# Performance work log

Measured on AMD Instinct MI355X. Metric: run time of the kernel, lower is better.

The kernel has to match this reference:

```python
import jax, jax.numpy as jnp
import numpy as np

B, T, E, H, DL, CC, K = 64, 2048, 512, 128, 1024, 32, 31


def setup_inputs() -> dict:
    key = jax.random.key(0)
    ks = jax.random.split(key, 8)
    return {
        "encoder_output": jax.random.normal(ks[0], (B, T, E), jnp.float32),
        "processed_encoder_output": jax.random.normal(ks[1], (B, T, H), jnp.float32),
        "lstm_output": jax.random.normal(ks[2], (B, 1, DL), jnp.float32),
        "attention_weights_cum": jax.random.uniform(ks[3], (B, T), jnp.float32),
        # learned params (torch Linear stores [out, in]; y = x @ W.T)
        "W_lstm": jax.random.normal(ks[4], (H, DL), jnp.float32) * 0.02,
        "conv_w": jax.random.normal(ks[5], (CC, 1, K), jnp.float32) * 0.1,
        "W_loc": jax.random.normal(ks[6], (H, CC), jnp.float32) * 0.1,
        "W_e": jax.random.normal(ks[7], (1, H), jnp.float32) * 0.1,
    }


def _forward(encoder_output, processed_encoder_output, lstm_output,
             attention_weights_cum, W_lstm, conv_w, W_loc, W_e):
    # [B,1,1024] @ [1024,128] -> [B,1,128]
    processed_lstm = jnp.einsum('bqd,hd->bqh', lstm_output, W_lstm)
    # location conv: [B,1,T] -> [B,32,T], same padding
    loc = lax.conv_general_dilated(
        attention_weights_cum[:, None, :], conv_w,
        window_strides=(1,), padding=[(K // 2, K // 2)],
        dimension_numbers=('NCH', 'OIH', 'NCH'))
    # transpose to [B,T,32] then dense to [B,T,128]
    processed_attn = jnp.einsum('bct,hc->bth', loc, W_loc)
    # additive energies: [B,T,128] -> [B,T]
    energies = jnp.einsum('bth,oh->bto',
                          jnp.tanh(processed_lstm + processed_attn + processed_encoder_output),
                          W_e)[..., 0]
    attention_weights = jax.nn.softmax(energies, axis=1)  # [B,T]
    # bmm: [B,1,T] @ [B,T,E] -> [B,1,E]
    attention_context = jnp.einsum('bt,bte->be', attention_weights, encoder_output)[:, None, :]
    return attention_context, attention_weights

from jax import lax


def reference(encoder_output, processed_encoder_output, lstm_output,
              attention_weights_cum, W_lstm, conv_w, W_loc, W_e):
    return _forward(encoder_output, processed_encoder_output, lstm_output,
                    attention_weights_cum, W_lstm, conv_w, W_loc, W_e)
```

## Files before the change

### kernel.cpp

```cpp
#include <hip/hip_runtime.h>
#include <math.h>


#define BB 64
#define TT 2048
#define EE 512
#define HH 128
#define DLL 1024
#define CCC 32
#define KK 31

#define WS_FW   0
#define WS_PL   4096
#define WS_EN   12288
#define WS_ST   143360
#define WS_PART 145472

__global__ __launch_bounds__(256) void k0_prep(const float* __restrict__ lstm,
                                               const float* __restrict__ Wl,
                                               const float* __restrict__ cw,
                                               const float* __restrict__ Wloc,
                                               float* __restrict__ ws) {
  const int blk = blockIdx.x;
  const int tid = threadIdx.x;
  if (blk < 2048) {
    const int wave = tid >> 6, lane = tid & 63;
    const int wg = blk * 4 + wave;
    const int b = wg >> 7, h = wg & 127;
    const float4* wr = (const float4*)(Wl + (size_t)h * DLL);
    const float4* lr = (const float4*)(lstm + (size_t)b * DLL);
    float s = 0.f;
#pragma unroll
    for (int m = 0; m < 4; ++m) {
      float4 a = wr[m * 64 + lane];
      float4 c = lr[m * 64 + lane];
      s += a.x * c.x + a.y * c.y + a.z * c.z + a.w * c.w;
    }
#pragma unroll
    for (int m = 1; m < 64; m <<= 1) s += __shfl_xor(s, m, 64);
    if (lane == 0) ws[WS_PL + b * HH + h] = s;
  } else {
    __shared__ __align__(16) float wl_s[HH * CCC];
    __shared__ __align__(16) float cw_s[CCC * KK];
#pragma unroll
    for (int m = 0; m < 4; ++m)
      ((float4*)wl_s)[tid + 256 * m] = ((const float4*)Wloc)[tid + 256 * m];
    if (tid < 248) ((float4*)cw_s)[tid] = ((const float4*)cw)[tid];
    __syncthreads();
    const int h = tid >> 1;
    const int kbase = (tid & 1) * 16;
    const int kn = (tid & 1) ? 15 : 16;
    for (int kk = 0; kk < kn; ++kk) {
      const int k = kbase + kk;
      float s = 0.f;
#pragma unroll
      for (int c = 0; c < CCC; ++c) s += wl_s[h * CCC + c] * cw_s[c * KK + k];
      ws[WS_FW + h * 32 + k] = s;
    }
    if (tid & 1) ws[WS_FW + h * 32 + 31] = 0.f;
  }
}

__global__ __launch_bounds__(256) void k1_fused(const float* __restrict__ pe,
                                                const float* __restrict__ aw,
                                                const float* __restrict__ We,
                                                const float* __restrict__ enc,
                                                float* __restrict__ ws) {
  const int b = blockIdx.y;
  const int chunk = blockIdx.x;
  const int t0 = chunk * 128;
  const int tid = threadIdx.x;
  const int wave = tid >> 6, lane = tid & 63;

  __shared__ __align__(16) float aw_s[160];
  __shared__ __align__(16) float e_s[128];
  __shared__ __align__(16) float w_chunk[128];
  __shared__ __align__(16) float4 acc_s[128];
  __shared__ float sm[4], ss[4], mb_s;

  if (tid < 160) {
    const int tg = t0 - 16 + tid;
    aw_s[tid] = (tg >= 0 && tg < TT) ? aw[b * TT + tg] : 0.f;
  }

  const int h0 = 2 * lane;
  float fw0[32], fw1[32];
  {
    const float4* f4 = (const float4*)(ws + WS_FW);
#pragma unroll
    for (int m = 0; m < 8; ++m) {
      float4 a = f4[h0 * 8 + m];
      fw0[4 * m + 0] = a.x; fw0[4 * m + 1] = a.y;
      fw0[4 * m + 2] = a.z; fw0[4 * m + 3] = a.w;
      float4 c = f4[h0 * 8 + 8 + m];
      fw1[4 * m + 0] = c.x; fw1[4 * m + 1] = c.y;
      fw1[4 * m + 2] = c.z; fw1[4 * m + 3] = c.w;
    }
  }
  const float2 plv = ((const float2*)(ws + WS_PL + b * HH))[lane];
  const float2 wev = ((const float2*)We)[lane];
  const float2* pe2 = (const float2*)(pe + (size_t)b * TT * HH);

  __syncthreads();

  float om = -3.4e38f, os = 0.f;

  for (int p = 0; p < 8; ++p) {
    const int tq = wave * 32 + p * 4;
    float2 pv[4];
#pragma unroll
    for (int j = 0; j < 4; ++j)
      pv[j] = pe2[(size_t)(t0 + tq + j) * 64 + lane];

    float w[36];
    const float4* a4 = (const float4*)&aw_s[tq];
#pragma unroll
    for (int m = 0; m < 9; ++m) {
      float4 v = a4[m];
      w[4 * m + 0] = v.x; w[4 * m + 1] = v.y;
      w[4 * m + 2] = v.z; w[4 * m + 3] = v.w;
    }

    float a0[4], a1[4];
#pragma unroll
    for (int j = 0; j < 4; ++j) {
      a0[j] = plv.x + pv[j].x;
      a1[j] = plv.y + pv[j].y;
    }
#pragma unroll
    for (int k = 0; k < 31; ++k) {
      const float f0 = fw0[k], f1 = fw1[k];
#pragma unroll
      for (int j = 0; j < 4; ++j) {
        a0[j] = fmaf(f0, w[1 + j + k], a0[j]);
        a1[j] = fmaf(f1, w[1 + j + k], a1[j]);
      }
    }
    float e[4];
#pragma unroll
    for (int j = 0; j < 4; ++j) {
      const float th0 = 1.f - 2.f / (__expf(2.f * a0[j]) + 1.f);
      const float th1 = 1.f - 2.f / (__expf(2.f * a1[j]) + 1.f);
      e[j] = wev.x * th0 + wev.y * th1;
    }
#pragma unroll
    for (int m = 1; m < 64; m <<= 1) {
#pragma unroll
      for (int j = 0; j < 4; ++j) e[j] += __shfl_xor(e[j], m, 64);
    }
    if (lane == 0) {
      const float4 ev = make_float4(e[0], e[1], e[2], e[3]);
      *(float4*)&e_s[tq] = ev;
      *(float4*)&ws[WS_EN + b * TT + t0 + tq] = ev;
    }
    float mq = fmaxf(fmaxf(e[0], e[1]), fmaxf(e[2], e[3]));
    float mn = fmaxf(om, mq);
    os = os * __expf(om - mn) + __expf(e[0] - mn) + __expf(e[1] - mn) +
         __expf(e[2] - mn) + __expf(e[3] - mn);
    om = mn;
  }

  if (lane == 0) { sm[wave] = om; ss[wave] = os; }
  __syncthreads();
  if (tid == 0) {
    const float mb = fmaxf(fmaxf(sm[0], sm[1]), fmaxf(sm[2], sm[3]));
    const float sb = ss[0] * __expf(sm[0] - mb) + ss[1] * __expf(sm[1] - mb) +
                     ss[2] * __expf(sm[2] - mb) + ss[3] * __expf(sm[3] - mb);
    float* st = ws + WS_ST + (b * 16 + chunk) * 2;
    st[0] = mb;
    st[1] = sb;
    mb_s = mb;
  }
  __syncthreads();
  if (tid < 128) w_chunk[tid] = __expf(e_s[tid] - mb_s);
  __syncthreads();

  const float4* enc4 = (const float4*)(enc + ((size_t)b * TT + t0) * EE);
  const int tp = tid >> 7;
  const int e4 = tid & 127;
  float4 acc0 = {0.f, 0.f, 0.f, 0.f}, acc1 = {0.f, 0.f, 0.f, 0.f};
#pragma unroll 8
  for (int i = 0; i < 64; ++i) {
    const int t = tp + 2 * i;
    const float w = w_chunk[t];
    const float4 v = enc4[(size_t)t * 128 + e4];
    if (i & 1) {
      acc1.x = fmaf(w, v.x, acc1.x); acc1.y = fmaf(w, v.y, acc1.y);
      acc1.z = fmaf(w, v.z, acc1.z); acc1.w = fmaf(w, v.w, acc1.w);
    } else {
      acc0.x = fmaf(w, v.x, acc0.x); acc0.y = fmaf(w, v.y, acc0.y);
      acc0.z = fmaf(w, v.z, acc0.z); acc0.w = fmaf(w, v.w, acc0.w);
    }
  }
  acc0.x += acc1.x; acc0.y += acc1.y; acc0.z += acc1.z; acc0.w += acc1.w;
  if (tp == 1) acc_s[e4] = acc0;
  __syncthreads();
  if (tp == 0) {
    const float4 o = acc_s[e4];
    acc0.x += o.x; acc0.y += o.y; acc0.z += o.z; acc0.w += o.w;
    ((float4*)(ws + WS_PART))[(size_t)(b * 16 + chunk) * 128 + e4] = acc0;
  }
}

__global__ __launch_bounds__(256) void k2_combine(const float* __restrict__ ws,
                                                  float* __restrict__ wts,
                                                  float* __restrict__ ctx) {
  const int b = blockIdx.x;
  const int tid = threadIdx.x;

  const float* st = ws + WS_ST + b * 32;
  float mb = -3.4e38f;
#pragma unroll
  for (int c = 0; c < 16; ++c) mb = fmaxf(mb, st[2 * c]);
  float S = 0.f;
#pragma unroll
  for (int c = 0; c < 16; ++c) S += st[2 * c + 1] * __expf(st[2 * c] - mb);
  const float inv = 1.f / S;

  __shared__ float esc[16];
  if (tid < 16) esc[tid] = __expf(st[2 * tid] - mb) * inv;
  __syncthreads();

  const float4* en4 = (const float4*)(ws + WS_EN + (size_t)b * TT);
  float4* w4 = (float4*)(wts + (size_t)b * TT);
#pragma unroll
  for (int j = 0; j < 2; ++j) {
    const float4 e = en4[tid * 2 + j];
    float4 w;
    w.x = __expf(e.x - mb) * inv;
    w.y = __expf(e.y - mb) * inv;
    w.z = __expf(e.z - mb) * inv;
    w.w = __expf(e.w - mb) * inv;
    w4[tid * 2 + j] = w;
  }

  const float2* p2 = (const float2*)(ws + WS_PART) + (size_t)b * 16 * 256 + tid;
  float2 s = {0.f, 0.f};
#pragma unroll
  for (int c = 0; c < 16; ++c) {
    const float2 v = p2[c * 256];
    s.x = fmaf(esc[c], v.x, s.x);
    s.y = fmaf(esc[c], v.y, s.y);
  }
  ((float2*)ctx)[b * 256 + tid] = s;
}

extern "C" void kernel_launch(void* const* d_in, const int* in_sizes, int n_in,
                              void* d_out, int out_size, void* d_ws, size_t ws_size,
                              hipStream_t stream) {
  const float* enc  = (const float*)d_in[0];
  const float* pe   = (const float*)d_in[1];
  const float* lstm = (const float*)d_in[2];
  const float* awc  = (const float*)d_in[3];
  const float* Wl   = (const float*)d_in[4];
  const float* cw   = (const float*)d_in[5];
  const float* Wloc = (const float*)d_in[6];
  const float* We   = (const float*)d_in[7];

  float* out = (float*)d_out;
  float* ctx = out;
  float* wts = out + BB * EE;
  float* ws = (float*)d_ws;

  k0_prep<<<2049, 256, 0, stream>>>(lstm, Wl, cw, Wloc, ws);
  k1_fused<<<dim3(16, BB), 256, 0, stream>>>(pe, awc, We, enc, ws);
  k2_combine<<<BB, 256, 0, stream>>>(ws, wts, ctx);
}
```

Before: 87.66 us.

## Fuse context accumulation into energy loop with online softmax rescaling

The separate pass that re-read encoder rows after the chunk's softmax stats were known is removed. Each wave now loads its four encoder rows at the top of each energy iteration and accumulates a weighted context with flash-style online max rescaling, then combines per-wave partials through an 8 KB shared buffer. The goal is to overlap the big encoder stream with the conv/tanh compute and drop two block barriers. The cost is more register pressure from holding the prefetched float4 rows and the per-iteration rescale multiplies.

New measurement: 91.52 us. +4.4%, slower.

```diff
diff --git a/kernel.cpp b/kernel.cpp
--- a/kernel.cpp
+++ b/kernel.cpp
@@ -73,10 +73,8 @@
   const int wave = tid >> 6, lane = tid & 63;
 
   __shared__ __align__(16) float aw_s[160];
-  __shared__ __align__(16) float e_s[128];
-  __shared__ __align__(16) float w_chunk[128];
-  __shared__ __align__(16) float4 acc_s[128];
-  __shared__ float sm[4], ss[4], mb_s;
+  __shared__ __align__(16) float comb[2048];
+  __shared__ float sm[4], ss[4];
 
   if (tid < 160) {
     const int tg = t0 - 16 + tid;
@@ -100,13 +98,25 @@
   const float2 plv = ((const float2*)(ws + WS_PL + b * HH))[lane];
   const float2 wev = ((const float2*)We)[lane];
   const float2* pe2 = (const float2*)(pe + (size_t)b * TT * HH);
+  const float4* enc4 = (const float4*)(enc + ((size_t)b * TT + t0) * EE);
 
   __syncthreads();
 
   float om = -3.4e38f, os = 0.f;
-
+  float4 acc0 = {0.f, 0.f, 0.f, 0.f};
+  float4 acc1 = {0.f, 0.f, 0.f, 0.f};
+
+#pragma unroll 1
   for (int p = 0; p < 8; ++p) {
     const int tq = wave * 32 + p * 4;
+
+    float4 ev0[4], ev1[4];
+#pragma unroll
+    for (int j = 0; j < 4; ++j) {
+      ev0[j] = enc4[(size_t)(tq + j) * 128 + lane];
+      ev1[j] = enc4[(size_t)(tq + j) * 128 + 64 + lane];
+    }
+
     float2 pv[4];
 #pragma unroll
     for (int j = 0; j < 4; ++j)
@@ -148,57 +158,58 @@
 #pragma unroll
       for (int j = 0; j < 4; ++j) e[j] += __shfl_xor(e[j], m, 64);
     }
-    if (lane == 0) {
-      const float4 ev = make_float4(e[0], e[1], e[2], e[3]);
-      *(float4*)&e_s[tq] = ev;
-      *(float4*)&ws[WS_EN + b * TT + t0 + tq] = ev;
-    }
-    float mq = fmaxf(fmaxf(e[0], e[1]), fmaxf(e[2], e[3]));
-    float mn = fmaxf(om, mq);
-    os = os * __expf(om - mn) + __expf(e[0] - mn) + __expf(e[1] - mn) +
-         __expf(e[2] - mn) + __expf(e[3] - mn);
+    if (lane == 0)
+      *(float4*)&ws[WS_EN + b * TT + t0 + tq] = make_float4(e[0], e[1], e[2], e[3]);
+
+    const float mq = fmaxf(fmaxf(e[0], e[1]), fmaxf(e[2], e[3]));
+    const float mn = fmaxf(om, mq);
+    const float sc = __expf(om - mn);
+    float wj[4];
+#pragma unroll
+    for (int j = 0; j < 4; ++j) wj[j] = __expf(e[j] - mn);
+    os = os * sc + wj[0] + wj[1] + wj[2] + wj[3];
+    acc0.x *= sc; acc0.y *= sc; acc0.z *= sc; acc0.w *= sc;
+    acc1.x *= sc; acc1.y *= sc; acc1.z *= sc; acc1.w *= sc;
+#pragma unroll
+    for (int j = 0; j < 4; ++j) {
+      acc0.x = fmaf(wj[j], ev0[j].x, acc0.x);
+      acc0.y = fmaf(wj[j], ev0[j].y, acc0.y);
+      acc0.z = fmaf(wj[j], ev0[j].z, acc0.z);
+      acc0.w = fmaf(wj[j], ev0[j].w, acc0.w);
+      acc1.x = fmaf(wj[j], ev1[j].x, acc1.x);
+      acc1.y = fmaf(wj[j], ev1[j].y, acc1.y);
+      acc1.z = fmaf(wj[j], ev1[j].z, acc1.z);
+      acc1.w = fmaf(wj[j], ev1[j].w, acc1.w);
+    }
     om = mn;
   }
 
   if (lane == 0) { sm[wave] = om; ss[wave] = os; }
   __syncthreads();
+  const float mb = fmaxf(fmaxf(sm[0], sm[1]), fmaxf(sm[2], sm[3]));
+  const float scw = __expf(om - mb);
+  acc0.x *= scw; acc0.y *= scw; acc0.z *= scw; acc0.w *= scw;
+  acc1.x *= scw; acc1.y *= scw; acc1.z *= scw; acc1.w *= scw;
+  ((float4*)comb)[wave * 128 + lane] = acc0;
+  ((float4*)comb)[wave * 128 + 64 + lane] = acc1;
+  __syncthreads();
+  {
+    const float2* c2 = (const float2*)comb;
+    float2 s = c2[tid];
+#pragma unroll
+    for (int w2 = 1; w2 < 4; ++w2) {
+      const float2 v = c2[w2 * 256 + tid];
+      s.x += v.x;
+      s.y += v.y;
+    }
+    ((float2*)(ws + WS_PART))[(size_t)(b * 16 + chunk) * 256 + tid] = s;
+  }
   if (tid == 0) {
-    const float mb = fmaxf(fmaxf(sm[0], sm[1]), fmaxf(sm[2], sm[3]));
     const float sb = ss[0] * __expf(sm[0] - mb) + ss[1] * __expf(sm[1] - mb) +
                      ss[2] * __expf(sm[2] - mb) + ss[3] * __expf(sm[3] - mb);
     float* st = ws + WS_ST + (b * 16 + chunk) * 2;
     st[0] = mb;
     st[1] = sb;
-    mb_s = mb;
-  }
-  __syncthreads();
-  if (tid < 128) w_chunk[tid] = __expf(e_s[tid] - mb_s);
-  __syncthreads();
-
-  const float4* enc4 = (const float4*)(enc + ((size_t)b * TT + t0) * EE);
-  const int tp = tid >> 7;
-  const int e4 = tid & 127;
-  float4 acc0 = {0.f, 0.f, 0.f, 0.f}, acc1 = {0.f, 0.f, 0.f, 0.f};
-#pragma unroll 8
-  for (int i = 0; i < 64; ++i) {
-    const int t = tp + 2 * i;
-    const float w = w_chunk[t];
-    const float4 v = enc4[(size_t)t * 128 + e4];
-    if (i & 1) {
-      acc1.x = fmaf(w, v.x, acc1.x); acc1.y = fmaf(w, v.y, acc1.y);
-      acc1.z = fmaf(w, v.z, acc1.z); acc1.w = fmaf(w, v.w, acc1.w);
-    } else {
-      acc0.x = fmaf(w, v.x, acc0.x); acc0.y = fmaf(w, v.y, acc0.y);
-      acc0.z = fmaf(w, v.z, acc0.z); acc0.w = fmaf(w, v.w, acc0.w);
-    }
-  }
-  acc0.x += acc1.x; acc0.y += acc1.y; acc0.z += acc1.z; acc0.w += acc1.w;
-  if (tp == 1) acc_s[e4] = acc0;
-  __syncthreads();
-  if (tp == 0) {
-    const float4 o = acc_s[e4];
-    acc0.x += o.x; acc0.y += o.y; acc0.z += o.z; acc0.w += o.w;
-    ((float4*)(ws + WS_PART))[(size_t)(b * 16 + chunk) * 128 + e4] = acc0;
   }
 }
 
```

## Remap energy computation to one thread per timestep with 128-thread blocks

Applied to the files above, without the earlier changes.

The fused attention kernel now assigns one timestep per thread and loops over all 128 hidden units. Fused conv/dense weights are staged in shared memory, and the 32-tap window is held in registers. This removes the per-timestep cross-lane shuffle reductions and the extra block-level partial-sum merge, at the cost of halving threads per block. Each thread now reads a contiguous 512-byte row of processed_encoder_output, so the loads are uncoalesced and may hurt memory efficiency. The encoder weighted sum now has each thread cover all 128 timesteps for one float4 column.

New measurement: 86.50 us. No clear change (-1.3%).

```diff
diff --git a/kernel.cpp b/kernel.cpp
--- a/kernel.cpp
+++ b/kernel.cpp
@@ -61,7 +61,7 @@
   }
 }
 
-__global__ __launch_bounds__(256) void k1_fused(const float* __restrict__ pe,
+__global__ __launch_bounds__(128) void k1_fused(const float* __restrict__ pe,
                                                 const float* __restrict__ aw,
                                                 const float* __restrict__ We,
                                                 const float* __restrict__ enc,
@@ -72,119 +72,96 @@
   const int tid = threadIdx.x;
   const int wave = tid >> 6, lane = tid & 63;
 
+  __shared__ __align__(16) float fw_s[HH * 32];
   __shared__ __align__(16) float aw_s[160];
-  __shared__ __align__(16) float e_s[128];
-  __shared__ __align__(16) float w_chunk[128];
-  __shared__ __align__(16) float4 acc_s[128];
-  __shared__ float sm[4], ss[4], mb_s;
-
-  if (tid < 160) {
-    const int tg = t0 - 16 + tid;
+  __shared__ float pl_s[128];
+  __shared__ float we_s[128];
+  __shared__ float w_chunk[128];
+  __shared__ float sm[2], ss[2];
+
+  {
+    const float4* src = (const float4*)(ws + WS_FW);
+    float4* dst = (float4*)fw_s;
+#pragma unroll
+    for (int i = 0; i < 8; ++i) dst[tid + 128 * i] = src[tid + 128 * i];
+  }
+  {
+    int tg = t0 - 16 + tid;
     aw_s[tid] = (tg >= 0 && tg < TT) ? aw[b * TT + tg] : 0.f;
-  }
-
-  const int h0 = 2 * lane;
-  float fw0[32], fw1[32];
-  {
-    const float4* f4 = (const float4*)(ws + WS_FW);
-#pragma unroll
-    for (int m = 0; m < 8; ++m) {
-      float4 a = f4[h0 * 8 + m];
-      fw0[4 * m + 0] = a.x; fw0[4 * m + 1] = a.y;
-      fw0[4 * m + 2] = a.z; fw0[4 * m + 3] = a.w;
-      float4 c = f4[h0 * 8 + 8 + m];
-      fw1[4 * m + 0] = c.x; fw1[4 * m + 1] = c.y;
-      fw1[4 * m + 2] = c.z; fw1[4 * m + 3] = c.w;
-    }
-  }
-  const float2 plv = ((const float2*)(ws + WS_PL + b * HH))[lane];
-  const float2 wev = ((const float2*)We)[lane];
-  const float2* pe2 = (const float2*)(pe + (size_t)b * TT * HH);
-
-  __syncthreads();
-
-  float om = -3.4e38f, os = 0.f;
-
-  for (int p = 0; p < 8; ++p) {
-    const int tq = wave * 32 + p * 4;
-    float2 pv[4];
-#pragma unroll
-    for (int j = 0; j < 4; ++j)
-      pv[j] = pe2[(size_t)(t0 + tq + j) * 64 + lane];
-
-    float w[36];
-    const float4* a4 = (const float4*)&aw_s[tq];
-#pragma unroll
-    for (int m = 0; m < 9; ++m) {
-      float4 v = a4[m];
-      w[4 * m + 0] = v.x; w[4 * m + 1] = v.y;
-      w[4 * m + 2] = v.z; w[4 * m + 3] = v.w;
-    }
-
-    float a0[4], a1[4];
-#pragma unroll
-    for (int j = 0; j < 4; ++j) {
-      a0[j] = plv.x + pv[j].x;
-      a1[j] = plv.y + pv[j].y;
-    }
-#pragma unroll
-    for (int k = 0; k < 31; ++k) {
-      const float f0 = fw0[k], f1 = fw1[k];
-#pragma unroll
-      for (int j = 0; j < 4; ++j) {
-        a0[j] = fmaf(f0, w[1 + j + k], a0[j]);
-        a1[j] = fmaf(f1, w[1 + j + k], a1[j]);
+    if (tid < 32) {
+      tg = t0 + 112 + tid;
+      aw_s[128 + tid] = (tg >= 0 && tg < TT) ? aw[b * TT + tg] : 0.f;
+    }
+  }
+  pl_s[tid] = ws[WS_PL + b * HH + tid];
+  we_s[tid] = We[tid];
+  __syncthreads();
+
+  float wreg[32];
+#pragma unroll
+  for (int k = 0; k < 32; ++k) wreg[k] = aw_s[tid + 1 + k];
+
+  const float4* pr4 = (const float4*)(pe + ((size_t)b * TT + t0 + tid) * HH);
+  float e_acc = 0.f;
+
+#pragma unroll 1
+  for (int h0 = 0; h0 < 128; h0 += 16) {
+    float4 ptv[4];
+#pragma unroll
+    for (int i = 0; i < 4; ++i) ptv[i] = pr4[(h0 >> 2) + i];
+    float pts[16];
+#pragma unroll
+    for (int i = 0; i < 4; ++i) {
+      pts[4 * i + 0] = ptv[i].x; pts[4 * i + 1] = ptv[i].y;
+      pts[4 * i + 2] = ptv[i].z; pts[4 * i + 3] = ptv[i].w;
+    }
+#pragma unroll 2
+    for (int hh = 0; hh < 16; ++hh) {
+      const int h = h0 + hh;
+      const float4* fr = (const float4*)&fw_s[h * 32];
+      float a0 = pl_s[h] + pts[hh];
+      float a1 = 0.f;
+#pragma unroll
+      for (int q = 0; q < 8; ++q) {
+        const float4 f = fr[q];
+        a0 = fmaf(f.x, wreg[4 * q + 0], a0);
+        a1 = fmaf(f.y, wreg[4 * q + 1], a1);
+        a0 = fmaf(f.z, wreg[4 * q + 2], a0);
+        a1 = fmaf(f.w, wreg[4 * q + 3], a1);
       }
-    }
-    float e[4];
-#pragma unroll
-    for (int j = 0; j < 4; ++j) {
-      const float th0 = 1.f - 2.f / (__expf(2.f * a0[j]) + 1.f);
-      const float th1 = 1.f - 2.f / (__expf(2.f * a1[j]) + 1.f);
-      e[j] = wev.x * th0 + wev.y * th1;
-    }
-#pragma unroll
-    for (int m = 1; m < 64; m <<= 1) {
-#pragma unroll
-      for (int j = 0; j < 4; ++j) e[j] += __shfl_xor(e[j], m, 64);
-    }
-    if (lane == 0) {
-      const float4 ev = make_float4(e[0], e[1], e[2], e[3]);
-      *(float4*)&e_s[tq] = ev;
-      *(float4*)&ws[WS_EN + b * TT + t0 + tq] = ev;
-    }
-    float mq = fmaxf(fmaxf(e[0], e[1]), fmaxf(e[2], e[3]));
-    float mn = fmaxf(om, mq);
-    os = os * __expf(om - mn) + __expf(e[0] - mn) + __expf(e[1] - mn) +
-         __expf(e[2] - mn) + __expf(e[3] - mn);
-    om = mn;
-  }
-
-  if (lane == 0) { sm[wave] = om; ss[wave] = os; }
-  __syncthreads();
+      const float x = a0 + a1;
+      const float th = 1.f - 2.f / (__expf(2.f * x) + 1.f);
+      e_acc = fmaf(we_s[h], th, e_acc);
+    }
+  }
+
+  ws[WS_EN + b * TT + t0 + tid] = e_acc;
+
+  float m = e_acc;
+#pragma unroll
+  for (int s = 1; s < 64; s <<= 1) m = fmaxf(m, __shfl_xor(m, s, 64));
+  float p = __expf(e_acc - m);
+#pragma unroll
+  for (int s = 1; s < 64; s <<= 1) p += __shfl_xor(p, s, 64);
+  if (lane == 0) { sm[wave] = m; ss[wave] = p; }
+  __syncthreads();
+  const float mb = fmaxf(sm[0], sm[1]);
   if (tid == 0) {
-    const float mb = fmaxf(fmaxf(sm[0], sm[1]), fmaxf(sm[2], sm[3]));
-    const float sb = ss[0] * __expf(sm[0] - mb) + ss[1] * __expf(sm[1] - mb) +
-                     ss[2] * __expf(sm[2] - mb) + ss[3] * __expf(sm[3] - mb);
+    const float sb = ss[0] * __expf(sm[0] - mb) + ss[1] * __expf(sm[1] - mb);
     float* st = ws + WS_ST + (b * 16 + chunk) * 2;
     st[0] = mb;
     st[1] = sb;
-    mb_s = mb;
-  }
-  __syncthreads();
-  if (tid < 128) w_chunk[tid] = __expf(e_s[tid] - mb_s);
+  }
+  w_chunk[tid] = __expf(e_acc - mb);
   __syncthreads();
 
   const float4* enc4 = (const float4*)(enc + ((size_t)b * TT + t0) * EE);
-  const int tp = tid >> 7;
-  const int e4 = tid & 127;
   float4 acc0 = {0.f, 0.f, 0.f, 0.f}, acc1 = {0.f, 0.f, 0.f, 0.f};
 #pragma unroll 8
-  for (int i = 0; i < 64; ++i) {
-    const int t = tp + 2 * i;
+  for (int t = 0; t < 128; ++t) {
     const float w = w_chunk[t];
-    const float4 v = enc4[(size_t)t * 128 + e4];
-    if (i & 1) {
+    const float4 v = enc4[(size_t)t * 128 + tid];
+    if (t & 1) {
       acc1.x = fmaf(w, v.x, acc1.x); acc1.y = fmaf(w, v.y, acc1.y);
       acc1.z = fmaf(w, v.z, acc1.z); acc1.w = fmaf(w, v.w, acc1.w);
     } else {
@@ -193,13 +170,7 @@
     }
   }
   acc0.x += acc1.x; acc0.y += acc1.y; acc0.z += acc1.z; acc0.w += acc1.w;
-  if (tp == 1) acc_s[e4] = acc0;
-  __syncthreads();
-  if (tp == 0) {
-    const float4 o = acc_s[e4];
-    acc0.x += o.x; acc0.y += o.y; acc0.z += o.z; acc0.w += o.w;
-    ((float4*)(ws + WS_PART))[(size_t)(b * 16 + chunk) * 128 + e4] = acc0;
-  }
+  ((float4*)(ws + WS_PART))[(size_t)(b * 16 + chunk) * 128 + tid] = acc0;
 }
 
 __global__ __launch_bounds__(256) void k2_combine(const float* __restrict__ ws,
@@ -263,6 +234,6 @@
   float* ws = (float*)d_ws;
 
   k0_prep<<<2049, 256, 0, stream>>>(lstm, Wl, cw, Wloc, ws);
-  k1_fused<<<dim3(16, BB), 256, 0, stream>>>(pe, awc, We, enc, ws);
+  k1_fused<<<dim3(16, BB), 128, 0, stream>>>(pe, awc, We, enc, ws);
   k2_combine<<<BB, 256, 0, stream>>>(ws, wts, ctx);
 }
```
